# Kernel tuning notes

Hardware: AMD Instinct MI355X
Metric: run time of the kernel (lower is better)

The kernel has to match this reference:

```python
import jax, jax.numpy as jnp
import numpy as np

NUM_EMBEDDINGS = 1024
EMBEDDING_DIM = 256
COMMITMENT_COST = 0.25


def setup_inputs() -> dict:
    key = jax.random.key(0)
    k1, k2 = jax.random.split(key)
    z_e = jax.random.normal(k1, (64, EMBEDDING_DIM, 32, 32), dtype=jnp.float32)
    # codebook init: uniform(-1/K, 1/K), matching nn.Embedding init in the module
    emb = jax.random.uniform(k2, (NUM_EMBEDDINGS, EMBEDDING_DIM), dtype=jnp.float32,
                             minval=-1.0 / NUM_EMBEDDINGS, maxval=1.0 / NUM_EMBEDDINGS)
    return {"z_e": z_e, "emb": emb}


def reference(z_e, emb):
    B, D, H, W = z_e.shape
    K = emb.shape[0]
    z = jnp.transpose(z_e, (0, 2, 3, 1))          # [B,H,W,D]
    x = z.reshape(-1, D)                           # [N,D], N = B*H*W
    dists = (jnp.sum(x * x, axis=1, keepdims=True)
             + jnp.sum(emb * emb, axis=1)[None, :]
             - 2.0 * (x @ emb.T))
    idx = jnp.argmin(dists, axis=1)                # [N] int
    z_q = emb[idx].reshape(z.shape)                # [B,H,W,D]
    e_latent_loss = jnp.mean((jax.lax.stop_gradient(z_q) - z) ** 2)
    q_latent_loss = jnp.mean((z_q - jax.lax.stop_gradient(z)) ** 2)
    loss = q_latent_loss + COMMITMENT_COST * e_latent_loss
    # straight-through estimator
    z_q_st = z + jax.lax.stop_gradient(z_q - z)
    counts = jnp.bincount(idx, length=K).astype(z.dtype)
    avg_probs = counts / jnp.asarray(x.shape[0], z.dtype)
    perplexity = jnp.exp(-jnp.sum(avg_probs * jnp.log(avg_probs + 1e-10)))
    return jnp.transpose(z_q_st, (0, 3, 1, 2)), loss, perplexity, idx
```

## Files before the change

kernel.cpp:

```cpp
#include <hip/hip_runtime.h>
#include <hip/hip_fp16.h>
#include <stdint.h>


#define D_DIM   256
#define K_CODES 1024
#define N_ROWS  65536
#define N_ELEM  16777216
#define IDX_OFF 16777218
#define FLAG_MARGIN 1.5e-4f
#define AMB_CAP 65536
#define A_SCALE 16.0f
#define B_SCALE 4096.0f
#define INV_SCALE2 3.0517578125e-05f

typedef short short8 __attribute__((ext_vector_type(8)));
typedef _Float16 half8 __attribute__((ext_vector_type(8)));
typedef float f32x4  __attribute__((ext_vector_type(4)));

__device__ __forceinline__ unsigned int mono(float s) {
    unsigned int u = __float_as_uint(s);
    return (u & 0x80000000u) ? ~u : (u | 0x80000000u);
}
__device__ __forceinline__ float unmono(unsigned int u) {
    return __uint_as_float((u & 0x80000000u) ? (u & 0x7FFFFFFFu) : ~u);
}
__device__ __forceinline__ unsigned short f16_rne(float x) {
    return __half_as_ushort(__float2half(x));
}
__device__ __forceinline__ void gld16(const void* g, void* l) {
    __builtin_amdgcn_global_load_lds(
        (const __attribute__((address_space(1))) unsigned int*)g,
        (__attribute__((address_space(3))) unsigned int*)l, 16, 0, 0);
}

__launch_bounds__(256)
__global__ void prep_kernel(const float* __restrict__ z_e,
                            const float* __restrict__ emb,
                            unsigned short* __restrict__ A_hi,
                            float* __restrict__ xnorm,
                            float* __restrict__ enorm,
                            unsigned short* __restrict__ B_hi,
                            float* __restrict__ embT,
                            int* __restrict__ counts,
                            float* __restrict__ loss_sum,
                            int* __restrict__ amb_count) {
#pragma clang fp contract(off)
    __shared__ float T[32][257];
    __shared__ float H[32][2];
    const int bid = blockIdx.x;
    const int tid = threadIdx.x;

    if (bid < 4) {
        const int k = bid * 256 + tid;
        counts[k] = 0;
        if (bid == 0 && tid == 0) { *loss_sum = 0.f; *amb_count = 0; }
        const float* p = emb + (size_t)k * D_DIM;
        unsigned int* dstB = (unsigned int*)(B_hi + (size_t)k * D_DIM);
        float halfv[2];
        #pragma unroll
        for (int h = 0; h < 2; ++h) {
            float r[8];
            #pragma unroll
            for (int qq = 0; qq < 2; ++qq) {
                const float* qb = p + h * 128 + qq * 64;
                float4 ev[16];
                #pragma unroll
                for (int m = 0; m < 16; ++m)
                    ev[m] = *(const float4*)(qb + 4 * m);
                #pragma unroll
                for (int t = 0; t < 8; ++t) {
                    const float4 a = ev[2 * t], b = ev[2 * t + 1];
                    if (qq == 0 && t == 0) {
                        r[0] = a.x * a.x; r[1] = a.y * a.y; r[2] = a.z * a.z; r[3] = a.w * a.w;
                        r[4] = b.x * b.x; r[5] = b.y * b.y; r[6] = b.z * b.z; r[7] = b.w * b.w;
                    } else {
                        r[0] += a.x * a.x; r[1] += a.y * a.y; r[2] += a.z * a.z; r[3] += a.w * a.w;
                        r[4] += b.x * b.x; r[5] += b.y * b.y; r[6] += b.z * b.z; r[7] += b.w * b.w;
                    }
                }
                #pragma unroll
                for (int m = 0; m < 16; m += 2) {
                    const float4 a = ev[m], b = ev[m + 1];
                    unsigned int u0 = f16_rne(a.x * B_SCALE) | ((unsigned int)f16_rne(a.y * B_SCALE) << 16);
                    unsigned int u1 = f16_rne(a.z * B_SCALE) | ((unsigned int)f16_rne(a.w * B_SCALE) << 16);
                    unsigned int u2 = f16_rne(b.x * B_SCALE) | ((unsigned int)f16_rne(b.y * B_SCALE) << 16);
                    unsigned int u3 = f16_rne(b.z * B_SCALE) | ((unsigned int)f16_rne(b.w * B_SCALE) << 16);
                    *(uint4*)(dstB + (h * 64 + qq * 32 + 2 * m)) = make_uint4(u0, u1, u2, u3);
                }
                const int dbase = h * 128 + qq * 64;
                #pragma unroll
                for (int m = 0; m < 16; ++m) {
                    embT[(size_t)(dbase + 4 * m + 0) * K_CODES + k] = ev[m].x;
                    embT[(size_t)(dbase + 4 * m + 1) * K_CODES + k] = ev[m].y;
                    embT[(size_t)(dbase + 4 * m + 2) * K_CODES + k] = ev[m].z;
                    embT[(size_t)(dbase + 4 * m + 3) * K_CODES + k] = ev[m].w;
                }
            }
            halfv[h] = ((r[0] + r[1]) + (r[2] + r[3])) + ((r[4] + r[5]) + (r[6] + r[7]));
        }
        enorm[k] = halfv[0] + halfv[1];
        return;
    }

    const int bx = bid - 4;
    const int b = bx >> 5, hw0 = (bx & 31) << 5;
    const float* zb = z_e + (size_t)b * 262144 + hw0;
    #pragma unroll 4
    for (int it = 0; it < 8; ++it) {
        int flat = it * 256 + tid;
        int d = flat >> 3;
        int hw4 = (flat & 7) << 2;
        float4 v = *(const float4*)(zb + (size_t)d * 1024 + hw4);
        T[hw4 + 0][d] = v.x; T[hw4 + 1][d] = v.y;
        T[hw4 + 2][d] = v.z; T[hw4 + 3][d] = v.w;
    }
    __syncthreads();
    if (tid < 64) {
        int row = tid >> 1, h = tid & 1;
        const float* q = &T[row][h * 128];
        float r[8];
        #pragma unroll
        for (int j = 0; j < 8; ++j) { float x = q[j]; r[j] = x * x; }
        for (int i = 8; i < 128; i += 8)
            #pragma unroll
            for (int j = 0; j < 8; ++j) { float x = q[i + j]; r[j] = r[j] + x * x; }
        H[row][h] = ((r[0] + r[1]) + (r[2] + r[3])) + ((r[4] + r[5]) + (r[6] + r[7]));
    }
    __syncthreads();
    if (tid < 32) xnorm[b * 1024 + hw0 + tid] = H[tid][0] + H[tid][1];
    {
        int row = tid >> 3, seg8 = tid & 7;
        const float* src = &T[row][seg8 * 32];
        unsigned short* dst = A_hi + ((size_t)(b * 1024 + hw0 + row) * 256 + seg8 * 32);
        #pragma unroll
        for (int c = 0; c < 4; ++c) {
            unsigned int ub[4];
            #pragma unroll
            for (int p = 0; p < 4; ++p) {
                unsigned int lo = f16_rne(src[c * 8 + 2 * p] * A_SCALE);
                unsigned int hi = f16_rne(src[c * 8 + 2 * p + 1] * A_SCALE);
                ub[p] = lo | (hi << 16);
            }
            *(uint4*)(dst + c * 8) = make_uint4(ub[0], ub[1], ub[2], ub[3]);
        }
    }
}

#define DSTEP(T, CUR, W0, W1, I0, I1)                                                   \
  {                                                                                     \
    const int t_ = (T);                                                                 \
    if (t_ + 2 < 64) {                                                                  \
      const int nc_ = (t_ + 2) >> 3, ns_ = (t_ + 2) & 7;                                \
      I0 = *(const uint4*)(B_hi + (((size_t)(nc_ * 128 + arsub)) << 8) + ns_ * 32 + aq);      \
      I1 = *(const uint4*)(B_hi + (((size_t)(nc_ * 128 + 64 + arsub)) << 8) + ns_ * 32 + aq); \
    }                                                                                   \
    __builtin_amdgcn_sched_barrier(0);                                                  \
    const char* bb_ = smem + 65536 + ((CUR) << 13);                                     \
    const int sv_ = t_ & 7;                                                             \
    half8 af[4], bf[4];                                                                 \
    _Pragma("unroll") for (int i = 0; i < 4; ++i)                                       \
      af[i] = *(const half8*)(smem + sv_ * 8192 + (wr * 64 + i * 16 + l16) * 64 + rdoff); \
    _Pragma("unroll") for (int j = 0; j < 4; ++j)                                       \
      bf[j] = *(const half8*)(bb_ + (wc * 64 + j * 16 + l16) * 64 + rdoff);             \
    __builtin_amdgcn_s_setprio(1);                                                      \
    _Pragma("unroll") for (int i = 0; i < 4; ++i)                                       \
      _Pragma("unroll") for (int j = 0; j < 4; ++j)                                     \
        acc[i][j] = __builtin_amdgcn_mfma_f32_16x16x32_f16(af[i], bf[j], acc[i][j], 0, 0, 0); \
    __builtin_amdgcn_s_setprio(0);                                                      \
    __builtin_amdgcn_sched_barrier(0);                                                  \
    if (t_ + 1 < 64) {                                                                  \
      char* nb_ = smem + 65536 + ((1 ^ (CUR)) << 13) + w * 1024 + (lane << 4);          \
      *(uint4*)nb_ = W0;                                                                \
      *(uint4*)(nb_ + 4096) = W1;                                                       \
    }                                                                                   \
    asm volatile("s_waitcnt lgkmcnt(0)" ::: "memory");                                  \
    __builtin_amdgcn_s_barrier();                                                       \
    __builtin_amdgcn_sched_barrier(0);                                                  \
  }

__launch_bounds__(256, 2)
__global__ void dist2_kernel(const unsigned short* __restrict__ A_hi,
                             const unsigned short* __restrict__ B_hi,
                             const float* __restrict__ xnorm,
                             const float* __restrict__ enorm,
                             int* __restrict__ fidx,
                             int* __restrict__ amb,
                             int* __restrict__ amb_count) {
    __shared__ __align__(16) char smem[81920];
    unsigned long long* red = (unsigned long long*)(smem + 65536);

    const int tid  = threadIdx.x;
    const int w = tid >> 6, lane = tid & 63;
    const int l16 = lane & 15, quad = lane >> 4;
    const int wc = w & 1, wr = w >> 1;
    const int row0 = blockIdx.x * 128;

    const int aq    = (((lane & 3) ^ ((lane >> 3) & 3)) << 3);
    const int arsub = (w << 4) + (lane >> 2);
    const int rdoff = ((quad ^ ((l16 >> 1) & 3)) << 4);

    #pragma unroll
    for (int t = 0; t < 16; ++t) {
        const int arow = ((t & 1) << 6) + arsub;
        const int s    = t >> 1;
        gld16(A_hi + (((size_t)(row0 + arow)) << 8) + s * 32 + aq,
              smem + t * 4096 + w * 1024);
    }
    uint4 p0, p1, q0, q1;
    p0 = *(const uint4*)(B_hi + (((size_t)(arsub)) << 8) + aq);
    p1 = *(const uint4*)(B_hi + (((size_t)(64 + arsub)) << 8) + aq);
    q0 = *(const uint4*)(B_hi + (((size_t)(arsub)) << 8) + 32 + aq);
    q1 = *(const uint4*)(B_hi + (((size_t)(64 + arsub)) << 8) + 32 + aq);
    {
        char* d0 = smem + 65536 + w * 1024 + (lane << 4);
        *(uint4*)d0 = p0;
        *(uint4*)(d0 + 4096) = p1;
    }
    asm volatile("s_waitcnt lgkmcnt(0)" ::: "memory");
    __builtin_amdgcn_s_barrier();
    __builtin_amdgcn_sched_barrier(0);

    float xnr[4][4];
    #pragma unroll
    for (int i = 0; i < 4; ++i)
        #pragma unroll
        for (int r = 0; r < 4; ++r)
            xnr[i][r] = xnorm[row0 + wr * 64 + i * 16 + quad * 4 + r];

    const float INF = __uint_as_float(0x7F800000u);
    float m1[4][4], m2[4][4];
    unsigned int ix[4][4];
    #pragma unroll
    for (int i = 0; i < 4; ++i)
        #pragma unroll
        for (int r = 0; r < 4; ++r) { m1[i][r] = INF; m2[i][r] = INF; ix[i][r] = 0u; }

    for (int cb = 0; cb < 8; ++cb) {
        f32x4 acc[4][4];
        #pragma unroll
        for (int i = 0; i < 4; ++i)
            #pragma unroll
            for (int j = 0; j < 4; ++j) acc[i][j] = (f32x4){0.f, 0.f, 0.f, 0.f};

        #pragma unroll
        for (int sh = 0; sh < 4; ++sh) {
            DSTEP(cb * 8 + 2 * sh,     0, q0, q1, p0, p1);
            DSTEP(cb * 8 + 2 * sh + 1, 1, p0, p1, q0, q1);
        }

        float enj[4];
        #pragma unroll
        for (int j = 0; j < 4; ++j) enj[j] = enorm[cb * 128 + wc * 64 + j * 16 + l16];
        #pragma unroll
        for (int i = 0; i < 4; ++i) {
            #pragma unroll
            for (int r = 0; r < 4; ++r) {
                const float xn = xnr[i][r];
                float a = m1[i][r], b = m2[i][r];
                unsigned int id = ix[i][r];
                #pragma unroll
                for (int j = 0; j < 4; ++j) {
                    const unsigned int n = cb * 128 + wc * 64 + j * 16 + l16;
                    float sc = fmaf(acc[i][j][r], -INV_SCALE2, xn + enj[j]);
                    bool c = sc < a;
                    b = fminf(b, fmaxf(a, sc));
                    a = fminf(a, sc);
                    id = c ? n : id;
                }
                m1[i][r] = a; m2[i][r] = b; ix[i][r] = id;
            }
        }
    }

    #pragma unroll
    for (int i = 0; i < 4; ++i) {
        #pragma unroll
        for (int r = 0; r < 4; ++r) {
            unsigned long long a1 = ((unsigned long long)mono(m1[i][r]) << 32) | ix[i][r];
            unsigned long long a2 = ((unsigned long long)mono(m2[i][r]) << 32) | 0xFFFFFFFFull;
            #pragma unroll
            for (int m = 1; m < 16; m <<= 1) {
                unsigned long long u1 = __shfl_xor(a1, m, 16);
                unsigned long long u2 = __shfl_xor(a2, m, 16);
                if (u1 < a1) { a2 = (a1 < u2) ? a1 : u2; a1 = u1; }
                else         { a2 = (a2 < u1) ? a2 : u1; }
            }
            if (l16 == 0) {
                int rowl = wr * 64 + i * 16 + quad * 4 + r;
                red[(rowl * 2 + wc) * 2 + 0] = a1;
                red[(rowl * 2 + wc) * 2 + 1] = a2;
            }
        }
    }
    __syncthreads();
    if (tid < 128) {
        unsigned long long a1 = red[(tid * 2 + 0) * 2 + 0];
        unsigned long long a2 = red[(tid * 2 + 0) * 2 + 1];
        unsigned long long b1 = red[(tid * 2 + 1) * 2 + 0];
        unsigned long long b2 = red[(tid * 2 + 1) * 2 + 1];
        if (b1 < a1) { a2 = (a1 < b2) ? a1 : b2; a1 = b1; }
        else         { a2 = (a2 < b1) ? a2 : b1; }
        const int row = row0 + tid;
        fidx[row] = (int)(a1 & 0xFFFFFFFFull);
        float s1 = unmono((unsigned int)(a1 >> 32));
        float s2 = unmono((unsigned int)(a2 >> 32));
        if (s2 - s1 <= FLAG_MARGIN) {
            int slot = atomicAdd(amb_count, 1);
            if (slot < AMB_CAP) amb[slot] = row;
        }
    }
}

__launch_bounds__(512)
__global__ void rescue4_kernel(const float* __restrict__ z_e,
                               const float* __restrict__ embT,
                               const float* __restrict__ xnorm,
                               const float* __restrict__ enorm,
                               const int* __restrict__ amb,
                               const int* __restrict__ amb_count,
                               int* __restrict__ fidx) {
    __shared__ float xs[4][256];
    __shared__ int rows[4];
    __shared__ unsigned long long pm[4][513];
    const int tid = threadIdx.x;
    int cnt = *amb_count;
    if (cnt > AMB_CAP) cnt = AMB_CAP;
    if (cnt <= 0) return;
    const int ngroups = (cnt + 3) >> 2;
    for (int g = blockIdx.x; g < ngroups; g += gridDim.x) {
        if (tid < 4) {
            int e = g * 4 + tid;
            rows[tid] = amb[e < cnt ? e : (cnt - 1)];
        }
        __syncthreads();
        {
            const int j = tid >> 7, d0 = (tid & 127) * 2;
            const int row = rows[j];
            const int b = row >> 10, hw = row & 1023;
            const float* zp = z_e + (size_t)b * 262144 + hw;
            xs[j][d0 + 0] = zp[(size_t)(d0 + 0) * 1024];
            xs[j][d0 + 1] = zp[(size_t)(d0 + 1) * 1024];
        }
        __syncthreads();

        double acc[2][4];
        #pragma unroll
        for (int c = 0; c < 2; ++c)
            #pragma unroll
            for (int j = 0; j < 4; ++j) acc[c][j] = 0.0;

        const float* ep = embT + 2 * tid;
        for (int d0 = 0; d0 < D_DIM; d0 += 8) {
            float2 ev[8];
            #pragma unroll
            for (int u = 0; u < 8; ++u)
                ev[u] = *(const float2*)(ep + (size_t)(d0 + u) * K_CODES);
            #pragma unroll
            for (int u = 0; u < 8; ++u) {
                const int d = d0 + u;
                double e0 = (double)ev[u].x, e1 = (double)ev[u].y;
                double x0 = (double)xs[0][d], x1 = (double)xs[1][d];
                double x2 = (double)xs[2][d], x3 = (double)xs[3][d];
                acc[0][0] += x0 * e0; acc[0][1] += x1 * e0; acc[0][2] += x2 * e0; acc[0][3] += x3 * e0;
                acc[1][0] += x0 * e1; acc[1][1] += x1 * e1; acc[1][2] += x2 * e1; acc[1][3] += x3 * e1;
            }
        }

        float xnr[4];
        #pragma unroll
        for (int j = 0; j < 4; ++j) xnr[j] = xnorm[rows[j]];

        unsigned long long mm[4] = {~0ull, ~0ull, ~0ull, ~0ull};
        #pragma unroll
        for (int c = 0; c < 2; ++c) {
            const int k = 2 * tid + c;
            const float en = enorm[k];
            #pragma unroll
            for (int j = 0; j < 4; ++j) {
                float dv = (float)acc[c][j];
                float t = xnr[j] + en;
                float s = t - 2.f * dv;
                unsigned long long p = ((unsigned long long)mono(s) << 32) | (unsigned int)k;
                if (p < mm[j]) mm[j] = p;
            }
        }
        #pragma unroll
        for (int j = 0; j < 4; ++j) pm[j][tid] = mm[j];
        __syncthreads();
        for (int s = 256; s > 0; s >>= 1) {
            if (tid < s) {
                #pragma unroll
                for (int j = 0; j < 4; ++j)
                    if (pm[j][tid + s] < pm[j][tid]) pm[j][tid] = pm[j][tid + s];
            }
            __syncthreads();
        }
        if (tid < 4) fidx[rows[tid]] = (int)(pm[tid][0] & 0xFFFFFFFFull);
        __syncthreads();
    }
}

__global__ void epilogue_kernel(const float* __restrict__ z_e,
                                const float* __restrict__ emb,
                                const int* __restrict__ fidx,
                                float* __restrict__ out,
                                int* __restrict__ counts,
                                float* __restrict__ loss_sum) {
    __shared__ int   kb[64];
    __shared__ float rs[256];
    const int tid = threadIdx.x;
    const int rcb = blockIdx.x;
    const int b   = rcb >> 4;
    const int hw0 = (rcb & 15) << 6;

    if (tid < 64) {
        int k = fidx[rcb * 64 + tid];
        kb[tid] = k;
        out[(size_t)IDX_OFF + (size_t)rcb * 64 + tid] = (float)k;
        atomicAdd(&counts[k], 1);
    }
    __syncthreads();

    const int j4 = (tid & 15) << 2;
    const int dq = tid >> 4;
    const float* e0 = emb + (size_t)kb[j4 + 0] * D_DIM;
    const float* e1 = emb + (size_t)kb[j4 + 1] * D_DIM;
    const float* e2 = emb + (size_t)kb[j4 + 2] * D_DIM;
    const float* e3 = emb + (size_t)kb[j4 + 3] * D_DIM;
    const size_t base = (size_t)b * 262144 + hw0 + j4;
    float ls = 0.f;
    #pragma unroll 4
    for (int d = dq; d < D_DIM; d += 16) {
        size_t off = base + ((size_t)d << 10);
        float4 x = *(const float4*)(z_e + off);
        float4 q;
        q.x = e0[d]; q.y = e1[d]; q.z = e2[d]; q.w = e3[d];
        *(float4*)(out + off) = q;
        float d0 = q.x - x.x, d1 = q.y - x.y, d2 = q.z - x.z, d3 = q.w - x.w;
        ls += d0 * d0; ls += d1 * d1; ls += d2 * d2; ls += d3 * d3;
    }
    rs[tid] = ls;
    __syncthreads();
    for (int s = 128; s > 0; s >>= 1) {
        if (tid < s) rs[tid] += rs[tid + s];
        __syncthreads();
    }
    if (tid == 0) atomicAdd(loss_sum, rs[0]);
}

__global__ void finalize_kernel(const int* __restrict__ counts,
                                const float* __restrict__ loss_sum,
                                float* __restrict__ out) {
    __shared__ float rs[256];
    const int tid = threadIdx.x;
    float s = 0.f;
    for (int k = tid; k < K_CODES; k += 256) {
        float p = (float)counts[k] / 65536.0f;
        s += p * logf(p + 1e-10f);
    }
    rs[tid] = s;
    __syncthreads();
    for (int st = 128; st > 0; st >>= 1) {
        if (tid < st) rs[tid] += rs[tid + st];
        __syncthreads();
    }
    if (tid == 0) {
        out[N_ELEM]     = loss_sum[0] * 1.25f / 16777216.0f;
        out[N_ELEM + 1] = expf(-rs[0]);
    }
}

extern "C" void kernel_launch(void* const* d_in, const int* in_sizes, int n_in,
                              void* d_out, int out_size, void* d_ws, size_t ws_size,
                              hipStream_t stream) {
    const float* z_e = (const float*)d_in[0];
    const float* emb = (const float*)d_in[1];
    float* out = (float*)d_out;
    char*  ws  = (char*)d_ws;

    unsigned short* A_hi = (unsigned short*)d_out;

    float*          enorm    = (float*)ws;
    float*          xnorm    = (float*)(ws + 4096);
    int*            fidx     = (int*)(ws + 266240);
    int*            counts   = (int*)(ws + 528384);
    float*          loss_sum = (float*)(ws + 532480);
    int*            amb_cnt  = (int*)(ws + 532484);
    int*            amb      = (int*)(ws + 532488);
    unsigned short* B_hi     = (unsigned short*)(ws + 794752);
    float*          embT     = (float*)(ws + 1319040);

    prep_kernel<<<2052, 256, 0, stream>>>(z_e, emb, A_hi, xnorm, enorm, B_hi, embT,
                                          counts, loss_sum, amb_cnt);
    dist2_kernel<<<512, 256, 0, stream>>>(A_hi, B_hi, xnorm, enorm, fidx, amb, amb_cnt);
    rescue4_kernel<<<1024, 512, 0, stream>>>(z_e, embT, xnorm, enorm, amb, amb_cnt, fidx);
    epilogue_kernel<<<N_ROWS / 64, 256, 0, stream>>>(z_e, emb, fidx, out, counts, loss_sum);
    finalize_kernel<<<1, 256, 0, stream>>>(counts, loss_sum, out);
}
```

Measured before the change: 270.9 us.

## Drop row-norm term in argmin, stage gathered codes in LDS, loosen scheduling

```diff
diff --git a/kernel.cpp b/kernel.cpp
--- a/kernel.cpp
+++ b/kernel.cpp
@@ -155,7 +155,6 @@
       I0 = *(const uint4*)(B_hi + (((size_t)(nc_ * 128 + arsub)) << 8) + ns_ * 32 + aq);      \
       I1 = *(const uint4*)(B_hi + (((size_t)(nc_ * 128 + 64 + arsub)) << 8) + ns_ * 32 + aq); \
     }                                                                                   \
-    __builtin_amdgcn_sched_barrier(0);                                                  \
     const char* bb_ = smem + 65536 + ((CUR) << 13);                                     \
     const int sv_ = t_ & 7;                                                             \
     half8 af[4], bf[4];                                                                 \
@@ -163,12 +162,9 @@
       af[i] = *(const half8*)(smem + sv_ * 8192 + (wr * 64 + i * 16 + l16) * 64 + rdoff); \
     _Pragma("unroll") for (int j = 0; j < 4; ++j)                                       \
       bf[j] = *(const half8*)(bb_ + (wc * 64 + j * 16 + l16) * 64 + rdoff);             \
-    __builtin_amdgcn_s_setprio(1);                                                      \
     _Pragma("unroll") for (int i = 0; i < 4; ++i)                                       \
       _Pragma("unroll") for (int j = 0; j < 4; ++j)                                     \
         acc[i][j] = __builtin_amdgcn_mfma_f32_16x16x32_f16(af[i], bf[j], acc[i][j], 0, 0, 0); \
-    __builtin_amdgcn_s_setprio(0);                                                      \
-    __builtin_amdgcn_sched_barrier(0);                                                  \
     if (t_ + 1 < 64) {                                                                  \
       char* nb_ = smem + 65536 + ((1 ^ (CUR)) << 13) + w * 1024 + (lane << 4);          \
       *(uint4*)nb_ = W0;                                                                \
@@ -176,13 +172,11 @@
     }                                                                                   \
     asm volatile("s_waitcnt lgkmcnt(0)" ::: "memory");                                  \
     __builtin_amdgcn_s_barrier();                                                       \
-    __builtin_amdgcn_sched_barrier(0);                                                  \
   }
 
 __launch_bounds__(256, 2)
 __global__ void dist2_kernel(const unsigned short* __restrict__ A_hi,
                              const unsigned short* __restrict__ B_hi,
-                             const float* __restrict__ xnorm,
                              const float* __restrict__ enorm,
                              int* __restrict__ fidx,
                              int* __restrict__ amb,
@@ -219,14 +213,6 @@
     }
     asm volatile("s_waitcnt lgkmcnt(0)" ::: "memory");
     __builtin_amdgcn_s_barrier();
-    __builtin_amdgcn_sched_barrier(0);
-
-    float xnr[4][4];
-    #pragma unroll
-    for (int i = 0; i < 4; ++i)
-        #pragma unroll
-        for (int r = 0; r < 4; ++r)
-            xnr[i][r] = xnorm[row0 + wr * 64 + i * 16 + quad * 4 + r];
 
     const float INF = __uint_as_float(0x7F800000u);
     float m1[4][4], m2[4][4];
@@ -256,13 +242,12 @@
         for (int i = 0; i < 4; ++i) {
             #pragma unroll
             for (int r = 0; r < 4; ++r) {
-                const float xn = xnr[i][r];
                 float a = m1[i][r], b = m2[i][r];
                 unsigned int id = ix[i][r];
                 #pragma unroll
                 for (int j = 0; j < 4; ++j) {
                     const unsigned int n = cb * 128 + wc * 64 + j * 16 + l16;
-                    float sc = fmaf(acc[i][j][r], -INV_SCALE2, xn + enj[j]);
+                    float sc = fmaf(acc[i][j][r], -INV_SCALE2, enj[j]);
                     bool c = sc < a;
                     b = fminf(b, fmaxf(a, sc));
                     a = fminf(a, sc);
@@ -401,6 +386,7 @@
     }
 }
 
+__launch_bounds__(256)
 __global__ void epilogue_kernel(const float* __restrict__ z_e,
                                 const float* __restrict__ emb,
                                 const int* __restrict__ fidx,
@@ -408,6 +394,7 @@
                                 int* __restrict__ counts,
                                 float* __restrict__ loss_sum) {
     __shared__ int   kb[64];
+    __shared__ float L[64][257];
     __shared__ float rs[256];
     const int tid = threadIdx.x;
     const int rcb = blockIdx.x;
@@ -422,12 +409,18 @@
     }
     __syncthreads();
 
+    #pragma unroll 4
+    for (int it = 0; it < 16; ++it) {
+        const int flat = it * 256 + tid;
+        const int row = flat >> 6, c4 = (flat & 63) << 2;
+        float4 v = *(const float4*)(emb + (size_t)kb[row] * D_DIM + c4);
+        L[row][c4 + 0] = v.x; L[row][c4 + 1] = v.y;
+        L[row][c4 + 2] = v.z; L[row][c4 + 3] = v.w;
+    }
+    __syncthreads();
+
     const int j4 = (tid & 15) << 2;
     const int dq = tid >> 4;
-    const float* e0 = emb + (size_t)kb[j4 + 0] * D_DIM;
-    const float* e1 = emb + (size_t)kb[j4 + 1] * D_DIM;
-    const float* e2 = emb + (size_t)kb[j4 + 2] * D_DIM;
-    const float* e3 = emb + (size_t)kb[j4 + 3] * D_DIM;
     const size_t base = (size_t)b * 262144 + hw0 + j4;
     float ls = 0.f;
     #pragma unroll 4
@@ -435,7 +428,8 @@
         size_t off = base + ((size_t)d << 10);
         float4 x = *(const float4*)(z_e + off);
         float4 q;
-        q.x = e0[d]; q.y = e1[d]; q.z = e2[d]; q.w = e3[d];
+        q.x = L[j4 + 0][d]; q.y = L[j4 + 1][d];
+        q.z = L[j4 + 2][d]; q.w = L[j4 + 3][d];
         *(float4*)(out + off) = q;
         float d0 = q.x - x.x, d1 = q.y - x.y, d2 = q.z - x.z, d3 = q.w - x.w;
         ls += d0 * d0; ls += d1 * d1; ls += d2 * d2; ls += d3 * d3;
@@ -493,7 +487,7 @@
 
     prep_kernel<<<2052, 256, 0, stream>>>(z_e, emb, A_hi, xnorm, enorm, B_hi, embT,
                                           counts, loss_sum, amb_cnt);
-    dist2_kernel<<<512, 256, 0, stream>>>(A_hi, B_hi, xnorm, enorm, fidx, amb, amb_cnt);
+    dist2_kernel<<<512, 256, 0, stream>>>(A_hi, B_hi, enorm, fidx, amb, amb_cnt);
     rescue4_kernel<<<1024, 512, 0, stream>>>(z_e, embT, xnorm, enorm, amb, amb_cnt, fidx);
     epilogue_kernel<<<N_ROWS / 64, 256, 0, stream>>>(z_e, emb, fidx, out, counts, loss_sum);
     finalize_kernel<<<1, 256, 0, stream>>>(counts, loss_sum, out);
```

New measurement: 259.6 us. 1.04x faster.
